# Performance work log

Measured on AMD Instinct MI355X. Metric: run time of the kernel, lower is better.

## Reference

```python
import jax, jax.numpy as jnp
import numpy as np

B, T, H = 2, 2048, 1024
NH = 16
HD = H // NH


def setup_inputs() -> dict:
    key = jax.random.key(0)
    ks = jax.random.split(key, 9)
    s = 0.02
    return {
        "x": jax.random.normal(ks[0], (B, T, H), dtype=jnp.float32),
        "attn_mask": jnp.ones((B, T), dtype=jnp.int32),
        "Wq": jax.random.normal(ks[1], (H, H), dtype=jnp.float32) * s,
        "bq": jnp.zeros((H,), dtype=jnp.float32),
        "Wk": jax.random.normal(ks[2], (H, H), dtype=jnp.float32) * s,
        "bk": jnp.zeros((H,), dtype=jnp.float32),
        "Wv": jax.random.normal(ks[3], (H, H), dtype=jnp.float32) * s,
        "bv": jnp.zeros((H,), dtype=jnp.float32),
        "Wo": jax.random.normal(ks[4], (H, H), dtype=jnp.float32) * s,
        "bo": jnp.zeros((H,), dtype=jnp.float32),
    }


def reference(x, attn_mask, Wq, bq, Wk, bk, Wv, bv, Wo, bo):
    Bc, Tc, Hc = x.shape
    scale = HD ** -0.5
    # projections; torch Linear: y = x @ W.T + b (here W stored as [in,out])
    q = (x @ Wq + bq).reshape(Bc, Tc, NH, HD).transpose(0, 2, 1, 3)  # [B,NH,T,HD]
    k = (x @ Wk + bk).reshape(Bc, Tc, NH, HD).transpose(0, 2, 1, 3)
    v = (x @ Wv + bv).reshape(Bc, Tc, NH, HD).transpose(0, 2, 1, 3)
    scores = jnp.einsum('bhqd,bhkd->bhqk', q, k) * scale  # [B,NH,T,T]
    mask = attn_mask.reshape(Bc, 1, 1, Tc)
    scores = jnp.where(mask == 0, jnp.float32(-jnp.inf), scores)
    probs = jax.nn.softmax(scores, axis=-1)
    ctx = jnp.einsum('bhqk,bhkd->bhqd', probs, v)  # [B,NH,T,HD]
    ctx = ctx.transpose(0, 2, 1, 3).reshape(Bc, Tc, Hc)
    out = ctx @ Wo + bo
    return out
```

## Files before the change

### kernel.cpp

```cpp
#include <hip/hip_runtime.h>

typedef _Float16 f16;
typedef _Float16 f16x8 __attribute__((ext_vector_type(8)));
typedef _Float16 f16x4 __attribute__((ext_vector_type(4)));
typedef __fp16 h16x2 __attribute__((ext_vector_type(2)));
typedef float f32x4 __attribute__((ext_vector_type(4)));

#define MFMA32(a, b, c) __builtin_amdgcn_mfma_f32_16x16x32_f16((a), (b), (c), 0, 0, 0)

static constexpr int Bb = 2, T = 2048, H = 1024, NH = 16, HD = 64;
static constexpr int M = Bb * T;
static constexpr int NQKV = 3 * H;
#define QSCALE 0.1803368801111f

__device__ __forceinline__ void gload_lds16(const void* g, void* l) {
  __builtin_amdgcn_global_load_lds(
      (const __attribute__((address_space(1))) void*)g,
      (__attribute__((address_space(3))) void*)l, 16, 0, 0);
}

__global__ __launch_bounds__(256) void pack_all(const float* __restrict__ x,
                                                const float* __restrict__ Wq,
                                                const float* __restrict__ Wk,
                                                const float* __restrict__ Wv,
                                                const float* __restrict__ Wo,
                                                const float* __restrict__ bq,
                                                const float* __restrict__ bk,
                                                const float* __restrict__ bv,
                                                const int* __restrict__ mask,
                                                f16* __restrict__ xh,
                                                f16* __restrict__ WqkvT,
                                                f16* __restrict__ WoT,
                                                float* __restrict__ bqkv,
                                                float* __restrict__ maskf) {
  __shared__ f16 tile[64][65];
  const int bid = blockIdx.x;
  if (bid < 4096) {
    int i = bid * 256 + threadIdx.x;
    float4 v = ((const float4*)x)[i];
    f16x4 o;
    o[0] = (f16)v.x; o[1] = (f16)v.y; o[2] = (f16)v.z; o[3] = (f16)v.w;
    *(f16x4*)(xh + (size_t)i * 4) = o;
  } else if (bid < 5120) {
    int t = bid - 4096;
    int z = t >> 8, rem = t & 255;
    const float* W = (z == 0) ? Wq : (z == 1) ? Wk : (z == 2) ? Wv : Wo;
    f16* Wt = (z < 3) ? (WqkvT + (size_t)z * H * H) : WoT;
    const float scale = (z == 0) ? QSCALE : 1.0f;
    int k0 = (rem >> 4) * 64, n0 = (rem & 15) * 64;
    for (int p = 0; p < 16; ++p) {
      int idx = threadIdx.x + p * 256;
      int r = idx >> 6, c = idx & 63;
      tile[r][c] = (f16)(W[(size_t)(k0 + r) * H + n0 + c] * scale);
    }
    __syncthreads();
    for (int p = 0; p < 16; ++p) {
      int idx = threadIdx.x + p * 256;
      int r = idx >> 6, c = idx & 63;
      Wt[(size_t)(n0 + r) * H + k0 + c] = tile[c][r];
    }
  } else if (bid < 5132) {
    int i = (bid - 5120) * 256 + threadIdx.x;
    if (i < 3072) {
      float v = (i < 1024) ? bq[i] * QSCALE : ((i < 2048) ? bk[i - 1024] : bv[i - 2048]);
      bqkv[i] = v;
    }
  } else {
    int i = (bid - 5132) * 256 + threadIdx.x;
    if (i < Bb * T) maskf[i] = mask[i] ? 1.0f : 0.0f;
  }
}

__global__ __launch_bounds__(256) void vtrans(const f16* __restrict__ QKV,
                                              f16* __restrict__ VT) {
  __shared__ f16 tile[64 * 64];
  const int tid = threadIdx.x;
  const int kv0 = blockIdx.x * 64, h = blockIdx.y, b = blockIdx.z;
  for (int p = 0; p < 2; ++p) {
    int idx = p * 256 + tid;
    int r = idx >> 3, gr = idx & 7;
    f16x8 v = *(const f16x8*)(QKV + (size_t)(b * T + kv0 + r) * NQKV + 2 * H + h * HD + gr * 8);
    *(f16x8*)&tile[r * 64 + (((gr + (r >> 3)) & 7) << 3)] = v;
  }
  __syncthreads();
  const size_t obase = ((size_t)(b * NH + h) * HD) * T + kv0;
  for (int p = 0; p < 2; ++p) {
    int idx = p * 256 + tid;
    int d = idx >> 3, kg = idx & 7;
    f16x8 v;
    for (int j = 0; j < 8; ++j) {
      int row = kg * 8 + j;
      v[j] = tile[row * 64 + ((((d >> 3) + kg) & 7) << 3) + (d & 7)];
    }
    *(f16x8*)(VT + obase + (size_t)d * T + kg * 8) = v;
  }
}

__device__ __forceinline__ f16x8 lds_frag(const f16* base, int row, int gr) {
  return *(const f16x8*)(base + row * 64 + ((gr ^ (row & 7)) << 3));
}

template <int TM, int TN, bool OUT_F32>
__global__ __launch_bounds__(256) void gemm_f16_bt(const f16* __restrict__ A,
                                                   const f16* __restrict__ Bt,
                                                   const float* __restrict__ bias,
                                                   void* __restrict__ Cout,
                                                   int Nn, int Kk) {
  __shared__ f16 As[TM * 64];
  __shared__ f16 Bs[TN * 64];
  const int tid = threadIdx.x;
  const int lane = tid & 63, w = tid >> 6;
  const int quad = lane >> 4, l16 = lane & 15;
  const int wm = w >> 1, wn = w & 1;
  const int m0 = blockIdx.y * TM, n0 = blockIdx.x * TN;
  constexpr int AM = TM / 32, AN = TN / 32;

  f32x4 acc[AM][AN];
  for (int a = 0; a < AM; ++a)
    for (int b2 = 0; b2 < AN; ++b2)
      for (int r = 0; r < 4; ++r) acc[a][b2][r] = 0.f;

  for (int k0 = 0; k0 < Kk; k0 += 64) {
    for (int p = 0; p < TM * 8 / 256; ++p) {
      int slot = p * 256 + w * 64 + lane;
      int r = slot >> 3, g = (slot & 7) ^ (r & 7);
      gload_lds16(A + (size_t)(m0 + r) * Kk + k0 + g * 8,
                  (char*)As + (p * 256 + w * 64) * 16);
    }
    for (int p = 0; p < TN * 8 / 256; ++p) {
      int slot = p * 256 + w * 64 + lane;
      int r = slot >> 3, g = (slot & 7) ^ (r & 7);
      gload_lds16(Bt + (size_t)(n0 + r) * Kk + k0 + g * 8,
                  (char*)Bs + (p * 256 + w * 64) * 16);
    }
    __syncthreads();
    for (int ks = 0; ks < 2; ++ks) {
      f16x8 af[AM], bf[AN];
      for (int t = 0; t < AM; ++t)
        af[t] = lds_frag(As, wm * (TM / 2) + t * 16 + l16, ks * 4 + quad);
      for (int t = 0; t < AN; ++t)
        bf[t] = lds_frag(Bs, wn * (TN / 2) + t * 16 + l16, ks * 4 + quad);
      for (int tm = 0; tm < AM; ++tm)
        for (int tn = 0; tn < AN; ++tn)
          acc[tm][tn] = MFMA32(af[tm], bf[tn], acc[tm][tn]);
    }
    __syncthreads();
  }

  for (int tm = 0; tm < AM; ++tm)
    for (int tn = 0; tn < AN; ++tn)
      for (int r = 0; r < 4; ++r) {
        int m = m0 + wm * (TM / 2) + tm * 16 + quad * 4 + r;
        int n = n0 + wn * (TN / 2) + tn * 16 + l16;
        float v = acc[tm][tn][r] + bias[n];
        if (OUT_F32)
          ((float*)Cout)[(size_t)m * Nn + n] = v;
        else
          ((f16*)Cout)[(size_t)m * Nn + n] = (f16)v;
      }
}


static constexpr int KT_ELE = 128 * 64;
static constexpr int VT_ELE = 64 * 128;

__global__ __launch_bounds__(512, 4) void attn_fused(const f16* __restrict__ QKV,
                                                     const f16* __restrict__ VT,
                                                     const float* __restrict__ maskf,
                                                     f16* __restrict__ ctx) {
  __shared__ char smem[(2 * KT_ELE + 2 * VT_ELE) * 2];
  f16* KtB = (f16*)smem;
  f16* VtB = (f16*)(smem + 2 * KT_ELE * 2);

  const int tid = threadIdx.x;
  const int w = tid >> 6, lane = tid & 63;
  const int quad = lane >> 4, l16 = lane & 15;
  const int qw = w & 3, g = w >> 2;
  const int q0 = blockIdx.x * 128, h = blockIdx.y, b = blockIdx.z;

  const size_t kbase = (size_t)(b * T) * NQKV + H + h * HD;
  const size_t vtbase = ((size_t)(b * NH + h) * HD) * T;
  const float* maskp = maskf + b * T;

  f16x8 qf[2][2];
  for (int tq = 0; tq < 2; ++tq) {
    const f16* qrow = QKV + (size_t)(b * T + q0 + qw * 32 + tq * 16 + l16) * NQKV + h * HD;
    qf[tq][0] = *(const f16x8*)(qrow + quad * 8);
    qf[tq][1] = *(const f16x8*)(qrow + 32 + quad * 8);
  }

  f32x4 oacc[2][4];
  float lsum[2] = {0.f, 0.f};
  for (int tq = 0; tq < 2; ++tq)
    for (int t = 0; t < 4; ++t)
      for (int r = 0; r < 4; ++r) oacc[tq][t][r] = 0.f;

  auto stage = [&](int kv0, int buf) {
    f16* Kd = KtB + buf * KT_ELE;
    f16* Vd = VtB + buf * VT_ELE;
    for (int p = 0; p < 2; ++p) {
      int s = p * 512 + tid;
      int R = s >> 3, sg = (s & 7) ^ (R & 7);
      int kv = (R & ~31) | ((R & 12) << 1) | ((R & 16) >> 2) | (R & 3);
      gload_lds16(QKV + kbase + (size_t)(kv0 + kv) * NQKV + sg * 8,
                  (char*)Kd + (p * 512 + w * 64) * 16);
    }
    for (int p = 0; p < 2; ++p) {
      int s = p * 512 + tid;
      int d = s >> 4, cg = s & 15;
      int kvl = (cg * 8 - 8 * (d & 15)) & 127;
      gload_lds16(VT + vtbase + (size_t)d * T + kv0 + kvl,
                  (char*)Vd + (p * 512 + w * 64) * 16);
    }
  };

  stage(0, 0);
  __syncthreads();

  for (int it = 0; it < T / 128; ++it) {
    const int cur = it & 1, nxt = cur ^ 1;
    if (it + 1 < T / 128) stage((it + 1) * 128, nxt);

    const f16* Kc = KtB + cur * KT_ELE;
    const f16* Vc = VtB + cur * VT_ELE;

    for (int s = 0; s < 2; ++s) {
      const int bi = g * 2 + s;
      const int kvabs = it * 128 + bi * 32;
      float4 m0 = *(const float4*)(maskp + kvabs + quad * 8);
      float4 m1 = *(const float4*)(maskp + kvabs + quad * 8 + 4);
      f16x8 kfA0 = lds_frag(Kc, bi * 32 + l16, quad);
      f16x8 kfA1 = lds_frag(Kc, bi * 32 + l16, 4 + quad);
      f16x8 kfB0 = lds_frag(Kc, bi * 32 + 16 + l16, quad);
      f16x8 kfB1 = lds_frag(Kc, bi * 32 + 16 + l16, 4 + quad);
      f16x8 vf[4];
      for (int td = 0; td < 4; ++td)
        vf[td] = *(const f16x8*)&Vc[(td * 16 + l16) * 128 +
                                    ((bi * 32 + quad * 8 + 8 * l16) & 127)];
      for (int tq = 0; tq < 2; ++tq) {
        f32x4 sA = {0.f, 0.f, 0.f, 0.f}, sB = {0.f, 0.f, 0.f, 0.f};
        sA = MFMA32(kfA0, qf[tq][0], sA);
        sA = MFMA32(kfA1, qf[tq][1], sA);
        sB = MFMA32(kfB0, qf[tq][0], sB);
        sB = MFMA32(kfB1, qf[tq][1], sB);
        float pA0 = __builtin_amdgcn_exp2f(sA[0]) * m0.x;
        float pA1 = __builtin_amdgcn_exp2f(sA[1]) * m0.y;
        float pA2 = __builtin_amdgcn_exp2f(sA[2]) * m0.z;
        float pA3 = __builtin_amdgcn_exp2f(sA[3]) * m0.w;
        float pB0 = __builtin_amdgcn_exp2f(sB[0]) * m1.x;
        float pB1 = __builtin_amdgcn_exp2f(sB[1]) * m1.y;
        float pB2 = __builtin_amdgcn_exp2f(sB[2]) * m1.z;
        float pB3 = __builtin_amdgcn_exp2f(sB[3]) * m1.w;
        lsum[tq] += ((pA0 + pA1) + (pA2 + pA3)) + ((pB0 + pB1) + (pB2 + pB3));
        union PF { f16x8 v; h16x2 h[4]; } pf;
        pf.h[0] = __builtin_amdgcn_cvt_pkrtz(pA0, pA1);
        pf.h[1] = __builtin_amdgcn_cvt_pkrtz(pA2, pA3);
        pf.h[2] = __builtin_amdgcn_cvt_pkrtz(pB0, pB1);
        pf.h[3] = __builtin_amdgcn_cvt_pkrtz(pB2, pB3);
        for (int td = 0; td < 4; ++td)
          oacc[tq][td] = MFMA32(vf[td], pf.v, oacc[tq][td]);
      }
    }
    __syncthreads();
  }

  float* cmb = (float*)smem;
  const int slot = qw * 64 + lane;
  if (g == 1) {
    float* dst = cmb + slot * 35;
    int i = 0;
    for (int tq = 0; tq < 2; ++tq)
      for (int td = 0; td < 4; ++td)
        for (int r = 0; r < 4; ++r) dst[i++] = oacc[tq][td][r];
    dst[32] = lsum[0];
    dst[33] = lsum[1];
  }
  __syncthreads();
  if (g == 0) {
    const float* src = cmb + slot * 35;
    int i = 0;
    for (int tq = 0; tq < 2; ++tq)
      for (int td = 0; td < 4; ++td)
        for (int r = 0; r < 4; ++r) oacc[tq][td][r] += src[i++];
    lsum[0] += src[32];
    lsum[1] += src[33];

    for (int tq = 0; tq < 2; ++tq) {
      float l = lsum[tq];
      l += __shfl_xor(l, 16, 64);
      l += __shfl_xor(l, 32, 64);
      float inv = 1.f / l;
      int row = b * T + q0 + qw * 32 + tq * 16 + l16;
      for (int td = 0; td < 4; ++td) {
        f16x4 o;
        for (int r = 0; r < 4; ++r) o[r] = (f16)(oacc[tq][td][r] * inv);
        *(f16x4*)(ctx + (size_t)row * H + h * HD + td * 16 + quad * 4) = o;
      }
    }
  }
}


extern "C" void kernel_launch(void* const* d_in, const int* in_sizes, int n_in,
                              void* d_out, int out_size, void* d_ws, size_t ws_size,
                              hipStream_t stream) {
  const float* x  = (const float*)d_in[0];
  const int* mask = (const int*)d_in[1];
  const float* Wq = (const float*)d_in[2];
  const float* bq = (const float*)d_in[3];
  const float* Wk = (const float*)d_in[4];
  const float* bk = (const float*)d_in[5];
  const float* Wv = (const float*)d_in[6];
  const float* bv = (const float*)d_in[7];
  const float* Wo = (const float*)d_in[8];
  const float* bo = (const float*)d_in[9];
  float* out = (float*)d_out;

  char* ws = (char*)d_ws;
  f16* xh      = (f16*)(ws);
  f16* Wqkv_t  = (f16*)(ws + (8u  << 20));
  f16* Wot     = (f16*)(ws + (14u << 20));
  float* bqkv  = (float*)(ws + (16u << 20));
  float* maskf = (float*)(ws + (16u << 20) + 65536);
  f16* QKV     = (f16*)(ws + (17u << 20));
  f16* ctx     = (f16*)(ws + (42u << 20));
  f16* VTr     = (f16*)(ws + (50u << 20));

  pack_all<<<dim3(5164), 256, 0, stream>>>(x, Wq, Wk, Wv, Wo, bq, bk, bv, mask,
                                           xh, Wqkv_t, Wot, bqkv, maskf);

  gemm_f16_bt<128, 128, false><<<dim3(NQKV / 128, M / 128), 256, 0, stream>>>(
      xh, Wqkv_t, bqkv, QKV, NQKV, H);

  vtrans<<<dim3(T / 64, NH, Bb), 256, 0, stream>>>(QKV, VTr);

  attn_fused<<<dim3(T / 128, NH, Bb), 512, 0, stream>>>(QKV, VTr, maskf, ctx);

  gemm_f16_bt<128, 64, true><<<dim3(H / 64, M / 128), 256, 0, stream>>>(
      ctx, Wot, bo, out, H, H);
}
```

Baseline: 209.9 us.

## Double-buffer GEMM LDS, widen attention query tile, pre-swizzle V in transpose

The GEMM kernel now uses two LDS buffers and prefetches the next K-slice while computing on the current one, so global loads overlap with MFMA work. The attention kernel handles 256 query rows per block instead of 128, with four query sub-tiles per wave. This reuses each staged K/V tile across twice as many queries, but halves the grid to 256 blocks and raises register pressure. The V rotation swizzle moves from the attention loader into the vtrans kernel's store, so attention issues plain contiguous loads.

```diff
diff --git a/kernel.cpp b/kernel.cpp
--- a/kernel.cpp
+++ b/kernel.cpp
@@ -83,7 +83,7 @@
     *(f16x8*)&tile[r * 64 + (((gr + (r >> 3)) & 7) << 3)] = v;
   }
   __syncthreads();
-  const size_t obase = ((size_t)(b * NH + h) * HD) * T + kv0;
+  const size_t obase = ((size_t)(b * NH + h) * HD) * T;
   for (int p = 0; p < 2; ++p) {
     int idx = p * 256 + tid;
     int d = idx >> 3, kg = idx & 7;
@@ -92,7 +92,9 @@
       int row = kg * 8 + j;
       v[j] = tile[row * 64 + ((((d >> 3) + kg) & 7) << 3) + (d & 7)];
     }
-    *(f16x8*)(VT + obase + (size_t)d * T + kg * 8) = v;
+    int kvr = kv0 + kg * 8;
+    int c = (kvr & ~127) | ((kvr + 8 * (d & 15)) & 127);
+    *(f16x8*)(VT + obase + (size_t)d * T + c) = v;
   }
 }
 
@@ -101,13 +103,13 @@
 }
 
 template <int TM, int TN, bool OUT_F32>
-__global__ __launch_bounds__(256) void gemm_f16_bt(const f16* __restrict__ A,
-                                                   const f16* __restrict__ Bt,
-                                                   const float* __restrict__ bias,
-                                                   void* __restrict__ Cout,
-                                                   int Nn, int Kk) {
-  __shared__ f16 As[TM * 64];
-  __shared__ f16 Bs[TN * 64];
+__global__ __launch_bounds__(256, 2) void gemm_f16_bt(const f16* __restrict__ A,
+                                                      const f16* __restrict__ Bt,
+                                                      const float* __restrict__ bias,
+                                                      void* __restrict__ Cout,
+                                                      int Nn, int Kk) {
+  __shared__ f16 As[2][TM * 64];
+  __shared__ f16 Bs[2][TN * 64];
   const int tid = threadIdx.x;
   const int lane = tid & 63, w = tid >> 6;
   const int quad = lane >> 4, l16 = lane & 15;
@@ -120,26 +122,33 @@
     for (int b2 = 0; b2 < AN; ++b2)
       for (int r = 0; r < 4; ++r) acc[a][b2][r] = 0.f;
 
-  for (int k0 = 0; k0 < Kk; k0 += 64) {
+  auto stage = [&](int k0, int buf) {
     for (int p = 0; p < TM * 8 / 256; ++p) {
       int slot = p * 256 + w * 64 + lane;
       int r = slot >> 3, g = (slot & 7) ^ (r & 7);
       gload_lds16(A + (size_t)(m0 + r) * Kk + k0 + g * 8,
-                  (char*)As + (p * 256 + w * 64) * 16);
+                  (char*)&As[buf][0] + (p * 256 + w * 64) * 16);
     }
     for (int p = 0; p < TN * 8 / 256; ++p) {
       int slot = p * 256 + w * 64 + lane;
       int r = slot >> 3, g = (slot & 7) ^ (r & 7);
       gload_lds16(Bt + (size_t)(n0 + r) * Kk + k0 + g * 8,
-                  (char*)Bs + (p * 256 + w * 64) * 16);
-    }
-    __syncthreads();
+                  (char*)&Bs[buf][0] + (p * 256 + w * 64) * 16);
+    }
+  };
+
+  stage(0, 0);
+  __syncthreads();
+  const int NIT = Kk / 64;
+  for (int it = 0; it < NIT; ++it) {
+    const int cur = it & 1;
+    if (it + 1 < NIT) stage((it + 1) * 64, cur ^ 1);
     for (int ks = 0; ks < 2; ++ks) {
       f16x8 af[AM], bf[AN];
       for (int t = 0; t < AM; ++t)
-        af[t] = lds_frag(As, wm * (TM / 2) + t * 16 + l16, ks * 4 + quad);
+        af[t] = lds_frag(&As[cur][0], wm * (TM / 2) + t * 16 + l16, ks * 4 + quad);
       for (int t = 0; t < AN; ++t)
-        bf[t] = lds_frag(Bs, wn * (TN / 2) + t * 16 + l16, ks * 4 + quad);
+        bf[t] = lds_frag(&Bs[cur][0], wn * (TN / 2) + t * 16 + l16, ks * 4 + quad);
       for (int tm = 0; tm < AM; ++tm)
         for (int tn = 0; tn < AN; ++tn)
           acc[tm][tn] = MFMA32(af[tm], bf[tn], acc[tm][tn]);
@@ -164,11 +173,11 @@
 static constexpr int KT_ELE = 128 * 64;
 static constexpr int VT_ELE = 64 * 128;
 
-__global__ __launch_bounds__(512, 4) void attn_fused(const f16* __restrict__ QKV,
+__global__ __launch_bounds__(512, 2) void attn_fused(const f16* __restrict__ QKV,
                                                      const f16* __restrict__ VT,
                                                      const float* __restrict__ maskf,
                                                      f16* __restrict__ ctx) {
-  __shared__ char smem[(2 * KT_ELE + 2 * VT_ELE) * 2];
+  __shared__ __align__(16) char smem[70656];
   f16* KtB = (f16*)smem;
   f16* VtB = (f16*)(smem + 2 * KT_ELE * 2);
 
@@ -176,22 +185,22 @@
   const int w = tid >> 6, lane = tid & 63;
   const int quad = lane >> 4, l16 = lane & 15;
   const int qw = w & 3, g = w >> 2;
-  const int q0 = blockIdx.x * 128, h = blockIdx.y, b = blockIdx.z;
+  const int q0 = blockIdx.x * 256, h = blockIdx.y, b = blockIdx.z;
 
   const size_t kbase = (size_t)(b * T) * NQKV + H + h * HD;
   const size_t vtbase = ((size_t)(b * NH + h) * HD) * T;
   const float* maskp = maskf + b * T;
 
-  f16x8 qf[2][2];
-  for (int tq = 0; tq < 2; ++tq) {
-    const f16* qrow = QKV + (size_t)(b * T + q0 + qw * 32 + tq * 16 + l16) * NQKV + h * HD;
+  f16x8 qf[4][2];
+  for (int tq = 0; tq < 4; ++tq) {
+    const f16* qrow = QKV + (size_t)(b * T + q0 + qw * 64 + tq * 16 + l16) * NQKV + h * HD;
     qf[tq][0] = *(const f16x8*)(qrow + quad * 8);
     qf[tq][1] = *(const f16x8*)(qrow + 32 + quad * 8);
   }
 
-  f32x4 oacc[2][4];
-  float lsum[2] = {0.f, 0.f};
-  for (int tq = 0; tq < 2; ++tq)
+  f32x4 oacc[4][4];
+  float lsum[4] = {0.f, 0.f, 0.f, 0.f};
+  for (int tq = 0; tq < 4; ++tq)
     for (int t = 0; t < 4; ++t)
       for (int r = 0; r < 4; ++r) oacc[tq][t][r] = 0.f;
 
@@ -208,8 +217,7 @@
     for (int p = 0; p < 2; ++p) {
       int s = p * 512 + tid;
       int d = s >> 4, cg = s & 15;
-      int kvl = (cg * 8 - 8 * (d & 15)) & 127;
-      gload_lds16(VT + vtbase + (size_t)d * T + kv0 + kvl,
+      gload_lds16(VT + vtbase + (size_t)d * T + kv0 + cg * 8,
                   (char*)Vd + (p * 512 + w * 64) * 16);
     }
   };
@@ -218,8 +226,8 @@
   __syncthreads();
 
   for (int it = 0; it < T / 128; ++it) {
-    const int cur = it & 1, nxt = cur ^ 1;
-    if (it + 1 < T / 128) stage((it + 1) * 128, nxt);
+    const int cur = it & 1;
+    if (it + 1 < T / 128) stage((it + 1) * 128, cur ^ 1);
 
     const f16* Kc = KtB + cur * KT_ELE;
     const f16* Vc = VtB + cur * VT_ELE;
@@ -237,7 +245,7 @@
       for (int td = 0; td < 4; ++td)
         vf[td] = *(const f16x8*)&Vc[(td * 16 + l16) * 128 +
                                     ((bi * 32 + quad * 8 + 8 * l16) & 127)];
-      for (int tq = 0; tq < 2; ++tq) {
+      for (int tq = 0; tq < 4; ++tq) {
         f32x4 sA = {0.f, 0.f, 0.f, 0.f}, sB = {0.f, 0.f, 0.f, 0.f};
         sA = MFMA32(kfA0, qf[tq][0], sA);
         sA = MFMA32(kfA1, qf[tq][1], sA);
@@ -267,30 +275,28 @@
   float* cmb = (float*)smem;
   const int slot = qw * 64 + lane;
   if (g == 1) {
-    float* dst = cmb + slot * 35;
+    float* dst = cmb + slot * 69;
     int i = 0;
-    for (int tq = 0; tq < 2; ++tq)
+    for (int tq = 0; tq < 4; ++tq)
       for (int td = 0; td < 4; ++td)
         for (int r = 0; r < 4; ++r) dst[i++] = oacc[tq][td][r];
-    dst[32] = lsum[0];
-    dst[33] = lsum[1];
+    for (int tq = 0; tq < 4; ++tq) dst[64 + tq] = lsum[tq];
   }
   __syncthreads();
   if (g == 0) {
-    const float* src = cmb + slot * 35;
+    const float* src = cmb + slot * 69;
     int i = 0;
-    for (int tq = 0; tq < 2; ++tq)
+    for (int tq = 0; tq < 4; ++tq)
       for (int td = 0; td < 4; ++td)
         for (int r = 0; r < 4; ++r) oacc[tq][td][r] += src[i++];
-    lsum[0] += src[32];
-    lsum[1] += src[33];
-
-    for (int tq = 0; tq < 2; ++tq) {
+    for (int tq = 0; tq < 4; ++tq) lsum[tq] += src[64 + tq];
+
+    for (int tq = 0; tq < 4; ++tq) {
       float l = lsum[tq];
       l += __shfl_xor(l, 16, 64);
       l += __shfl_xor(l, 32, 64);
       float inv = 1.f / l;
-      int row = b * T + q0 + qw * 32 + tq * 16 + l16;
+      int row = b * T + q0 + qw * 64 + tq * 16 + l16;
       for (int td = 0; td < 4; ++td) {
         f16x4 o;
         for (int r = 0; r < 4; ++r) o[r] = (f16)(oacc[tq][td][r] * inv);
@@ -334,7 +340,7 @@
 
   vtrans<<<dim3(T / 64, NH, Bb), 256, 0, stream>>>(QKV, VTr);
 
-  attn_fused<<<dim3(T / 128, NH, Bb), 512, 0, stream>>>(QKV, VTr, maskf, ctx);
+  attn_fused<<<dim3(T / 256, NH, Bb), 512, 0, stream>>>(QKV, VTr, maskf, ctx);
 
   gemm_f16_bt<128, 64, true><<<dim3(H / 64, M / 128), 256, 0, stream>>>(
       ctx, Wot, bo, out, H, H);
```

Result: faster. 195.9 us (-6.7%).
